# Kernel tuning notes

Hardware: AMD Instinct MI355X
Metric: run time of the kernel (lower is better)

Reference implementation:

```python
import jax, jax.numpy as jnp
import numpy as np

DECAY = 0.99   # LIF membrane decay
INH = 1.625    # lateral inhibition strength (mode='max')


def setup_inputs() -> dict:
    key = jax.random.key(0)
    kx, kw = jax.random.split(key)
    B, Cin, Cout = 8192, 4096, 1024
    x = (jax.random.uniform(kx, (B, Cin)) < 0.2).astype(jnp.float32)
    # weights, then normweight(): clamp to [0,1] and scale each row so row-max == 0.1
    W = jax.random.uniform(kw, (Cout, Cin), dtype=jnp.float32)
    W = W / (W.max(axis=1, keepdims=True) / 0.1)
    return {"x": x, "W": W, "time_window": 10}


def reference(x, W, time_window):
    # current through the bias-free linear layer; constant across timesteps
    i = x @ W.T                                   # (B, Cout)
    # adaptive threshold init: threshold = 3 * max over batch (thre_init branch)
    thr = 3.0 * i.max(axis=0)                     # (Cout,)
    imax = i.max(axis=1, keepdims=True)           # (B, 1), for mode='max' inhibition
    C = i.shape[1]

    def step(mem, _):
        mem = mem * DECAY + i                     # LIF integration
        s = (mem > thr).astype(i.dtype)           # threshold fire
        mem = mem * (1.0 - s)                     # hard reset at all spikers
        row = s.max(axis=1, keepdims=True)        # (B,1) 1 if any neuron in row spiked
        # winner-take-all k=1: keep a single spiking neuron per row (first/argmax)
        wta = jax.nn.one_hot(jnp.argmax(s, axis=1), C, dtype=i.dtype) * row
        # lateral inhibition: subtract inh * max-current from losers in rows that spiked
        mem = mem - INH * imax * (row - wta)
        return mem, wta

    mem0 = jnp.zeros_like(i)
    _, wtas = jax.lax.scan(step, mem0, None, length=time_window)
    return wtas.sum(axis=0)                       # accumulated spikes (B, Cout)
```

## Files before the change

kernel.cpp:

```cpp
#include <hip/hip_runtime.h>
#include <cstdint>

#define B_DIM 8192
#define CIN   4096
#define COUT  1024
#define NPLN  3072

constexpr double W_SCALE   = 83230720.0;
constexpr int    QMAX      = 8323072;
constexpr double INV_SCALE = 0.1 / 8323072.0;

using i32x4 = __attribute__((ext_vector_type(4))) int;

__device__ __forceinline__ void async_copy16(void* lds, const void* g) {
    auto l = (__attribute__((address_space(3))) void*)(uintptr_t)(lds);
    auto p = (const __attribute__((address_space(1))) void*)(uintptr_t)(g);
    __builtin_amdgcn_global_load_lds(p, l, 16, 0, 0);
}

__global__ void prep_x(const float* __restrict__ x, int8_t* __restrict__ Ai) {
    const int idx = blockIdx.x * 256 + threadIdx.x;
    const float4* xp = (const float4*)x + (size_t)idx * 4;
    float4 v0 = xp[0], v1 = xp[1], v2 = xp[2], v3 = xp[3];
    auto pk = [](float a, float b, float c, float d) -> int {
        return (a != 0.f ? 1 : 0) | ((b != 0.f ? 1 : 0) << 8) |
               ((c != 0.f ? 1 : 0) << 16) | ((d != 0.f ? 1 : 0) << 24);
    };
    int4 r;
    r.x = pk(v0.x, v0.y, v0.z, v0.w);
    r.y = pk(v1.x, v1.y, v1.z, v1.w);
    r.z = pk(v2.x, v2.y, v2.z, v2.w);
    r.w = pk(v3.x, v3.y, v3.z, v3.w);
    ((int4*)Ai)[idx] = r;
}

__global__ void prep_w(const float* __restrict__ W, int8_t* __restrict__ Bd,
                       unsigned long long* __restrict__ cm) {
    const int idx = blockIdx.x * 256 + threadIdx.x;
    float4 w = ((const float4*)W)[idx];
    float ws[4] = {w.x, w.y, w.z, w.w};
    char dg[3][4];
#pragma unroll
    for (int k = 0; k < 4; ++k) {
        int qv = __double2int_rn((double)ws[k] * W_SCALE);
        qv = max(0, min(QMAX, qv));
        int d0 = ((qv + 128) & 255) - 128; int tq = (qv - d0) >> 8;
        int d1 = ((tq + 128) & 255) - 128; int d2 = (tq - d1) >> 8;
        dg[0][k] = (char)d0; dg[1][k] = (char)d1; dg[2][k] = (char)d2;
    }
    const size_t off = (size_t)idx * 4;
#pragma unroll
    for (int p = 0; p < 3; ++p) {
        char4 c4; c4.x = dg[p][0]; c4.y = dg[p][1]; c4.z = dg[p][2]; c4.w = dg[p][3];
        *(char4*)(Bd + (size_t)p * COUT * CIN + off) = c4;
    }
    if (idx < COUT) cm[idx] = 0ull;
}

__global__ __launch_bounds__(256, 2) void gemm_i8(const int8_t* __restrict__ A,
                                                  const int8_t* __restrict__ Bm,
                                                  int* __restrict__ S) {
    __shared__ alignas(16) int8_t As[128 * 64];
    __shared__ alignas(16) int8_t Bs[128 * 64];
    const int tid  = threadIdx.x;
    const int lane = tid & 63;
    const int wave = tid >> 6;
    const int wr = wave >> 1, wc = wave & 1;
    const int bn = blockIdx.x, bm = blockIdx.y;

    const int r0  = tid >> 2;
    const int c0  = tid & 3;
    const int gc0 = c0 ^ ((r0 >> 1) & 3);
    const int r1  = r0 + 64;
    const int gc1 = c0 ^ ((r1 >> 1) & 3);
    const int8_t* Ag0 = A  + (size_t)(bm * 128 + r0) * CIN + gc0 * 16;
    const int8_t* Ag1 = A  + (size_t)(bm * 128 + r1) * CIN + gc1 * 16;
    const int8_t* Bg0 = Bm + (size_t)(bn * 128 + r0) * CIN + gc0 * 16;
    const int8_t* Bg1 = Bm + (size_t)(bn * 128 + r1) * CIN + gc1 * 16;
    int8_t* AsW = As + wave * 1024;
    int8_t* BsW = Bs + wave * 1024;

    const int mrow = lane & 15;
    const int q    = lane >> 4;
    const int sw   = (mrow >> 1) & 3;
    const int aoff = (wr * 64 + mrow) * 64 + (q ^ sw) * 16;
    const int boff = (wc * 64 + mrow) * 64 + (q ^ sw) * 16;

    i32x4 acc[4][4] = {};
    for (int kc = 0; kc < CIN; kc += 64) {
        __syncthreads();
        async_copy16(AsW,        Ag0 + kc);
        async_copy16(AsW + 4096, Ag1 + kc);
        async_copy16(BsW,        Bg0 + kc);
        async_copy16(BsW + 4096, Bg1 + kc);
        __syncthreads();
        i32x4 a[4], b[4];
#pragma unroll
        for (int t = 0; t < 4; ++t) a[t] = *(const i32x4*)(As + aoff + t * 1024);
#pragma unroll
        for (int t = 0; t < 4; ++t) b[t] = *(const i32x4*)(Bs + boff + t * 1024);
#pragma unroll
        for (int mt = 0; mt < 4; ++mt)
#pragma unroll
            for (int nt = 0; nt < 4; ++nt)
                acc[mt][nt] = __builtin_amdgcn_mfma_i32_16x16x64_i8(a[mt], b[nt], acc[mt][nt], 0, 0, 0);
    }

    const int gm0 = bm * 128 + wr * 64 + q * 4;
    const int gn0 = bn * 128 + wc * 64 + mrow;
#pragma unroll
    for (int mt = 0; mt < 4; ++mt)
#pragma unroll
        for (int nt = 0; nt < 4; ++nt) {
            const int gn = gn0 + nt * 16;
#pragma unroll
            for (int reg = 0; reg < 4; ++reg) {
                const int gm = gm0 + mt * 16 + reg;
                S[(size_t)gm * NPLN + gn] = acc[mt][nt][reg];
            }
        }
}

__global__ void colmax_k(const int* __restrict__ S, unsigned long long* __restrict__ cm) {
    const int j = blockIdx.x * 256 + threadIdx.x;
    const int rbeg = blockIdx.y * 128;
    double m = 0.0;
    for (int r = rbeg; r < rbeg + 128; ++r) {
        const int* row = S + (size_t)r * NPLN;
        long long s0 = row[j], s1 = row[COUT + j], s2 = row[2 * COUT + j];
        long long isum = s0 + s1 * 256 + s2 * 65536;
        double v = (double)isum * INV_SCALE;
        m = fmax(m, v);
    }
    atomicMax(cm + j, (unsigned long long)__double_as_longlong(m));
}

__global__ void scan_k(const int* __restrict__ S, const unsigned long long* __restrict__ cm,
                       const int* __restrict__ twp, float* __restrict__ out) {
    const int lane = threadIdx.x & 63;
    const int wave = threadIdx.x >> 6;
    const int b = blockIdx.x * 4 + wave;
    const int T = *twp;
    const int* row = S + (size_t)b * NPLN;

    double iv[16], mem[16], thr[16];
    int cnt[16];
    double imax = 0.0;
#pragma unroll
    for (int u = 0; u < 16; ++u) {
        const int j = lane + u * 64;
        long long s0 = row[j], s1 = row[COUT + j], s2 = row[2 * COUT + j];
        long long isum = s0 + s1 * 256 + s2 * 65536;
        iv[u]  = (double)isum * INV_SCALE;
        thr[u] = 3.0 * __longlong_as_double((long long)cm[j]);
        mem[u] = 0.0; cnt[u] = 0;
        imax = fmax(imax, iv[u]);
    }
#pragma unroll
    for (int d = 32; d >= 1; d >>= 1) imax = fmax(imax, __shfl_xor(imax, d, 64));
    const double h = 1.625 * imax;

    for (int t = 0; t < T; ++t) {
        int first = 0x7fffffff;
        bool sp[16];
#pragma unroll
        for (int u = 0; u < 16; ++u) {
            mem[u] = mem[u] * 0.99 + iv[u];
            sp[u] = mem[u] > thr[u];
            if (sp[u]) first = min(first, lane + u * 64);
        }
#pragma unroll
        for (int d = 32; d >= 1; d >>= 1) first = min(first, __shfl_xor(first, d, 64));
        const bool rowspike = first < 0x7fffffff;
#pragma unroll
        for (int u = 0; u < 16; ++u) {
            if (sp[u]) mem[u] = 0.0;
            if (rowspike) {
                if (lane + u * 64 == first) cnt[u]++;
                else mem[u] -= h;
            }
        }
    }
#pragma unroll
    for (int u = 0; u < 16; ++u)
        out[(size_t)b * COUT + lane + u * 64] = (float)cnt[u];
}

extern "C" void kernel_launch(void* const* d_in, const int* in_sizes, int n_in,
                              void* d_out, int out_size, void* d_ws, size_t ws_size,
                              hipStream_t stream) {
    const float* x  = (const float*)d_in[0];
    const float* W  = (const float*)d_in[1];
    const int*   tw = (const int*)d_in[2];
    float* out = (float*)d_out;

    int8_t* Ai = (int8_t*)d_ws;
    int8_t* Bd = Ai + (size_t)B_DIM * CIN;
    int*    S  = (int*)(Bd + (size_t)NPLN * CIN);
    unsigned long long* cm =
        (unsigned long long*)((int8_t*)S + (size_t)B_DIM * NPLN * 4);

    hipLaunchKernelGGL(prep_x,   dim3(8192),   dim3(256), 0, stream, x, Ai);
    hipLaunchKernelGGL(prep_w,   dim3(4096),   dim3(256), 0, stream, W, Bd, cm);
    hipLaunchKernelGGL(gemm_i8,  dim3(24, 64), dim3(256), 0, stream, Ai, Bd, S);
    hipLaunchKernelGGL(colmax_k, dim3(4, 64),  dim3(256), 0, stream, S, cm);
    hipLaunchKernelGGL(scan_k,   dim3(2048),   dim3(256), 0, stream, S, cm, tw, out);
}
```

Measured before the change: 391.6 us.

## Rewrite int8 GEMM with 256x256 tiles, double-buffered LDS pipeline and XCD-aware mapping

The int8 MFMA GEMM moves from 128x128 tiles with 4 waves and a load-then-compute loop to 256x256 tiles with 8 waves and 128-wide K chunks. A double-buffered 128KB LDS pipeline interleaves async global-to-LDS copies with MFMA quadrants, synchronised by explicit barriers, waitcnts and s_setprio. Workgroup ids are remapped across XCDs for L2 locality. The aim is to hide load latency and raise data reuse, at the cost of heavy LDS use, occupancy limits and fragile hand-counted waits.

After: 376.6 us. 1.04x faster.

```diff
diff --git a/kernel.cpp b/kernel.cpp
--- a/kernel.cpp
+++ b/kernel.cpp
@@ -57,68 +57,126 @@
     if (idx < COUT) cm[idx] = 0ull;
 }
 
-__global__ __launch_bounds__(256, 2) void gemm_i8(const int8_t* __restrict__ A,
+template <int MH, int NH>
+__device__ __forceinline__ void mma_quad(const i32x4 (&a)[4][2], const i32x4 (&b)[2][2],
+                                         i32x4 (&acc)[2][2][4][2]) {
+    __builtin_amdgcn_s_setprio(1);
+#pragma unroll
+    for (int mi = 0; mi < 4; ++mi)
+#pragma unroll
+        for (int ni = 0; ni < 2; ++ni)
+#pragma unroll
+            for (int kk = 0; kk < 2; ++kk)
+                acc[MH][NH][mi][ni] = __builtin_amdgcn_mfma_i32_16x16x64_i8(
+                    a[mi][kk], b[ni][kk], acc[MH][NH][mi][ni], 0, 0, 0);
+    __builtin_amdgcn_s_setprio(0);
+}
+
+#define BAR()   __builtin_amdgcn_s_barrier()
+#define LGKM0() asm volatile("s_waitcnt lgkmcnt(0)" ::: "memory")
+#define VMW(n)  asm volatile("s_waitcnt vmcnt(" #n ")" ::: "memory")
+
+__global__ __launch_bounds__(512, 2) void gemm_i8(const int8_t* __restrict__ A,
                                                   const int8_t* __restrict__ Bm,
                                                   int* __restrict__ S) {
-    __shared__ alignas(16) int8_t As[128 * 64];
-    __shared__ alignas(16) int8_t Bs[128 * 64];
+    __shared__ alignas(16) int8_t lds[131072];
     const int tid  = threadIdx.x;
     const int lane = tid & 63;
     const int wave = tid >> 6;
-    const int wr = wave >> 1, wc = wave & 1;
-    const int bn = blockIdx.x, bm = blockIdx.y;
-
-    const int r0  = tid >> 2;
-    const int c0  = tid & 3;
-    const int gc0 = c0 ^ ((r0 >> 1) & 3);
-    const int r1  = r0 + 64;
-    const int gc1 = c0 ^ ((r1 >> 1) & 3);
-    const int8_t* Ag0 = A  + (size_t)(bm * 128 + r0) * CIN + gc0 * 16;
-    const int8_t* Ag1 = A  + (size_t)(bm * 128 + r1) * CIN + gc1 * 16;
-    const int8_t* Bg0 = Bm + (size_t)(bn * 128 + r0) * CIN + gc0 * 16;
-    const int8_t* Bg1 = Bm + (size_t)(bn * 128 + r1) * CIN + gc1 * 16;
-    int8_t* AsW = As + wave * 1024;
-    int8_t* BsW = Bs + wave * 1024;
-
-    const int mrow = lane & 15;
-    const int q    = lane >> 4;
-    const int sw   = (mrow >> 1) & 3;
-    const int aoff = (wr * 64 + mrow) * 64 + (q ^ sw) * 16;
-    const int boff = (wc * 64 + mrow) * 64 + (q ^ sw) * 16;
-
-    i32x4 acc[4][4] = {};
-    for (int kc = 0; kc < CIN; kc += 64) {
-        __syncthreads();
-        async_copy16(AsW,        Ag0 + kc);
-        async_copy16(AsW + 4096, Ag1 + kc);
-        async_copy16(BsW,        Bg0 + kc);
-        async_copy16(BsW + 4096, Bg1 + kc);
-        __syncthreads();
-        i32x4 a[4], b[4];
-#pragma unroll
-        for (int t = 0; t < 4; ++t) a[t] = *(const i32x4*)(As + aoff + t * 1024);
-#pragma unroll
-        for (int t = 0; t < 4; ++t) b[t] = *(const i32x4*)(Bs + boff + t * 1024);
-#pragma unroll
-        for (int mt = 0; mt < 4; ++mt)
-#pragma unroll
-            for (int nt = 0; nt < 4; ++nt)
-                acc[mt][nt] = __builtin_amdgcn_mfma_i32_16x16x64_i8(a[mt], b[nt], acc[mt][nt], 0, 0, 0);
-    }
-
-    const int gm0 = bm * 128 + wr * 64 + q * 4;
-    const int gn0 = bn * 128 + wc * 64 + mrow;
-#pragma unroll
-    for (int mt = 0; mt < 4; ++mt)
-#pragma unroll
-        for (int nt = 0; nt < 4; ++nt) {
-            const int gn = gn0 + nt * 16;
-#pragma unroll
-            for (int reg = 0; reg < 4; ++reg) {
-                const int gm = gm0 + mt * 16 + reg;
-                S[(size_t)gm * NPLN + gn] = acc[mt][nt][reg];
-            }
-        }
+
+    const int wg = ((int)blockIdx.x & 7) * 48 + ((int)blockIdx.x >> 3);
+    const int bm = wg & 31;
+    const int bn = wg >> 5;
+
+    const int stid   = tid >> 3;
+    const int cswz16 = ((tid & 7) ^ (stid & 7)) << 4;
+    const int8_t* gA = A  + (size_t)(bm * 256 + stid) * CIN + cswz16;
+    const int8_t* gB = Bm + (size_t)(bn * 256 + stid) * CIN + cswz16;
+    const int wv1024 = wave << 10;
+
+#define STAGE_A(t_, hs_) do {                                                   \
+    int8_t* d_ = lds + (((t_) & 1) << 15) + ((hs_) << 14) + wv1024;             \
+    const int8_t* s_ = gA + (size_t)((hs_) * 128) * CIN + ((t_) << 7);          \
+    async_copy16(d_,        s_);                                                \
+    async_copy16(d_ + 8192, s_ + (size_t)64 * CIN);                             \
+} while (0)
+#define STAGE_B(t_, hs_) do {                                                   \
+    int8_t* d_ = lds + 65536 + (((t_) & 1) << 15) + ((hs_) << 14) + wv1024;     \
+    const int8_t* s_ = gB + (size_t)((hs_) * 128) * CIN + ((t_) << 7);          \
+    async_copy16(d_,        s_);                                                \
+    async_copy16(d_ + 8192, s_ + (size_t)64 * CIN);                             \
+} while (0)
+
+    const int wr = wave >> 2, wc = wave & 3;
+    const int fr = lane & 15;
+    const int q  = lane >> 4;
+    const int ck0 = (q ^ (lane & 7)) << 4;
+    const int ck1 = ck0 ^ 64;
+    const int abase = (wr * 64 + fr) * 128;
+    const int bbase = 65536 + (wc * 32 + fr) * 128;
+
+    i32x4 a[4][2], b0[2][2], b1[2][2];
+    i32x4 acc[2][2][4][2] = {};
+
+#define LDA(buf_, mh_) do {                                                     \
+    const int8_t* p_ = lds + ((buf_) << 15) + ((mh_) << 14) + abase;            \
+    a[0][0] = *(const i32x4*)(p_ + ck0);        a[0][1] = *(const i32x4*)(p_ + ck1);        \
+    a[1][0] = *(const i32x4*)(p_ + 2048 + ck0); a[1][1] = *(const i32x4*)(p_ + 2048 + ck1); \
+    a[2][0] = *(const i32x4*)(p_ + 4096 + ck0); a[2][1] = *(const i32x4*)(p_ + 4096 + ck1); \
+    a[3][0] = *(const i32x4*)(p_ + 6144 + ck0); a[3][1] = *(const i32x4*)(p_ + 6144 + ck1); \
+} while (0)
+#define LDB(arr_, buf_, nh_) do {                                               \
+    const int8_t* p_ = lds + ((buf_) << 15) + ((nh_) << 14) + bbase;            \
+    arr_[0][0] = *(const i32x4*)(p_ + ck0);        arr_[0][1] = *(const i32x4*)(p_ + ck1);        \
+    arr_[1][0] = *(const i32x4*)(p_ + 2048 + ck0); arr_[1][1] = *(const i32x4*)(p_ + 2048 + ck1); \
+} while (0)
+
+    STAGE_A(0, 0); STAGE_B(0, 0); STAGE_B(0, 1); STAGE_A(0, 1);
+    STAGE_A(1, 0); STAGE_B(1, 0);
+    VMW(8); BAR();
+
+#pragma unroll 1
+    for (int it = 0; it < 15; ++it) {
+        const int t = it * 2;
+        LDA(0, 0); LDB(b0, 0, 0); STAGE_B(t + 1, 1); BAR(); LGKM0(); mma_quad<0, 0>(a, b0, acc); VMW(8); BAR();
+        LDB(b1, 0, 1);            STAGE_A(t + 1, 1); BAR(); LGKM0(); mma_quad<0, 1>(a, b1, acc); VMW(8); BAR();
+        LDA(0, 1);                STAGE_A(t + 2, 0); BAR(); LGKM0(); mma_quad<1, 0>(a, b0, acc); VMW(8); BAR();
+                                  STAGE_B(t + 2, 0); BAR(); LGKM0(); mma_quad<1, 1>(a, b1, acc); VMW(8); BAR();
+        LDA(1, 0); LDB(b0, 1, 0); STAGE_B(t + 2, 1); BAR(); LGKM0(); mma_quad<0, 0>(a, b0, acc); VMW(8); BAR();
+        LDB(b1, 1, 1);            STAGE_A(t + 2, 1); BAR(); LGKM0(); mma_quad<0, 1>(a, b1, acc); VMW(8); BAR();
+        LDA(1, 1);                STAGE_A(t + 3, 0); BAR(); LGKM0(); mma_quad<1, 0>(a, b0, acc); VMW(8); BAR();
+                                  STAGE_B(t + 3, 0); BAR(); LGKM0(); mma_quad<1, 1>(a, b1, acc); VMW(8); BAR();
+    }
+    LDA(0, 0); LDB(b0, 0, 0); STAGE_B(31, 1); BAR(); LGKM0(); mma_quad<0, 0>(a, b0, acc); VMW(8); BAR();
+    LDB(b1, 0, 1);            STAGE_A(31, 1); BAR(); LGKM0(); mma_quad<0, 1>(a, b1, acc); VMW(8); BAR();
+    LDA(0, 1);                                BAR(); LGKM0(); mma_quad<1, 0>(a, b0, acc); VMW(8); BAR();
+                                              BAR(); LGKM0(); mma_quad<1, 1>(a, b1, acc); VMW(4); BAR();
+    LDA(1, 0); LDB(b0, 1, 0);                 BAR(); LGKM0(); mma_quad<0, 0>(a, b0, acc); VMW(2); BAR();
+    LDB(b1, 1, 1);                            BAR(); LGKM0(); mma_quad<0, 1>(a, b1, acc); VMW(0); BAR();
+    LDA(1, 1);                                BAR(); LGKM0(); mma_quad<1, 0>(a, b0, acc);
+                                                              mma_quad<1, 1>(a, b1, acc);
+
+    const int gm0 = bm * 256 + wr * 64 + q * 4;
+    const int gn0 = bn * 256 + wc * 32 + fr;
+#pragma unroll
+    for (int mh = 0; mh < 2; ++mh)
+#pragma unroll
+        for (int nh = 0; nh < 2; ++nh)
+#pragma unroll
+            for (int mi = 0; mi < 4; ++mi)
+#pragma unroll
+                for (int ni = 0; ni < 2; ++ni) {
+                    const int gn = gn0 + nh * 128 + ni * 16;
+#pragma unroll
+                    for (int reg = 0; reg < 4; ++reg) {
+                        const int gm = gm0 + mh * 128 + mi * 16 + reg;
+                        S[(size_t)gm * NPLN + gn] = acc[mh][nh][mi][ni][reg];
+                    }
+                }
+#undef STAGE_A
+#undef STAGE_B
+#undef LDA
+#undef LDB
 }
 
 __global__ void colmax_k(const int* __restrict__ S, unsigned long long* __restrict__ cm) {
@@ -200,9 +258,9 @@
     unsigned long long* cm =
         (unsigned long long*)((int8_t*)S + (size_t)B_DIM * NPLN * 4);
 
-    hipLaunchKernelGGL(prep_x,   dim3(8192),   dim3(256), 0, stream, x, Ai);
-    hipLaunchKernelGGL(prep_w,   dim3(4096),   dim3(256), 0, stream, W, Bd, cm);
-    hipLaunchKernelGGL(gemm_i8,  dim3(24, 64), dim3(256), 0, stream, Ai, Bd, S);
-    hipLaunchKernelGGL(colmax_k, dim3(4, 64),  dim3(256), 0, stream, S, cm);
-    hipLaunchKernelGGL(scan_k,   dim3(2048),   dim3(256), 0, stream, S, cm, tw, out);
-}
+    hipLaunchKernelGGL(prep_x,   dim3(8192),  dim3(256), 0, stream, x, Ai);
+    hipLaunchKernelGGL(prep_w,   dim3(4096),  dim3(256), 0, stream, W, Bd, cm);
+    hipLaunchKernelGGL(gemm_i8,  dim3(384),   dim3(512), 0, stream, Ai, Bd, S);
+    hipLaunchKernelGGL(colmax_k, dim3(4, 64), dim3(256), 0, stream, S, cm);
+    hipLaunchKernelGGL(scan_k,   dim3(2048),  dim3(256), 0, stream, S, cm, tw, out);
+}
```

## Fuse digit-plane recombination and column max into pipelined 512-thread int8 GEMM

Applied to the files above, without the earlier changes.

Rewrites the int8 GEMM so each 512-thread block computes a 128x256 output tile for all three weight digit planes, accumulating them in registers. Loads are double-buffered through 128KB of LDS with explicit waitcnt and barrier scheduling, and MFMA sections are wrapped in setprio. The epilogue recombines the planes into double values, writes a single double matrix, and folds the column max into the GEMM through an LDS reduction plus atomicMax, which removes the colmax kernel and the three-plane int32 intermediate. In exchange it adds register pressure (48 accumulator vectors) and a large LDS footprint that limits occupancy.

Result: faster. 345.5 us (-11.8%).

```diff
diff --git a/kernel.cpp b/kernel.cpp
--- a/kernel.cpp
+++ b/kernel.cpp
@@ -4,7 +4,6 @@
 #define B_DIM 8192
 #define CIN   4096
 #define COUT  1024
-#define NPLN  3072
 
 constexpr double W_SCALE   = 83230720.0;
 constexpr int    QMAX      = 8323072;
@@ -57,91 +56,160 @@
     if (idx < COUT) cm[idx] = 0ull;
 }
 
-__global__ __launch_bounds__(256, 2) void gemm_i8(const int8_t* __restrict__ A,
+template <int P>
+__device__ __forceinline__ void mma16(const i32x4 (&a)[4], const i32x4 (&b)[4],
+                                      i32x4 (&acc)[3][4][4]) {
+    __builtin_amdgcn_s_setprio(1);
+#pragma unroll
+    for (int mi = 0; mi < 4; ++mi)
+#pragma unroll
+        for (int ni = 0; ni < 4; ++ni)
+            acc[P][mi][ni] = __builtin_amdgcn_mfma_i32_16x16x64_i8(
+                a[mi], b[ni], acc[P][mi][ni], 0, 0, 0);
+    __builtin_amdgcn_s_setprio(0);
+}
+
+#define BAR()   __builtin_amdgcn_s_barrier()
+#define LGKM0() asm volatile("s_waitcnt lgkmcnt(0)" ::: "memory")
+#define VMW(n)  asm volatile("s_waitcnt vmcnt(" #n ")" ::: "memory")
+
+__global__ __launch_bounds__(512, 2) void gemm_i8(const int8_t* __restrict__ A,
                                                   const int8_t* __restrict__ Bm,
-                                                  int* __restrict__ S) {
-    __shared__ alignas(16) int8_t As[128 * 64];
-    __shared__ alignas(16) int8_t Bs[128 * 64];
+                                                  double* __restrict__ Sc,
+                                                  unsigned long long* __restrict__ cm) {
+    __shared__ alignas(16) int8_t lds[131072];
     const int tid  = threadIdx.x;
     const int lane = tid & 63;
     const int wave = tid >> 6;
-    const int wr = wave >> 1, wc = wave & 1;
-    const int bn = blockIdx.x, bm = blockIdx.y;
-
-    const int r0  = tid >> 2;
-    const int c0  = tid & 3;
-    const int gc0 = c0 ^ ((r0 >> 1) & 3);
-    const int r1  = r0 + 64;
-    const int gc1 = c0 ^ ((r1 >> 1) & 3);
-    const int8_t* Ag0 = A  + (size_t)(bm * 128 + r0) * CIN + gc0 * 16;
-    const int8_t* Ag1 = A  + (size_t)(bm * 128 + r1) * CIN + gc1 * 16;
-    const int8_t* Bg0 = Bm + (size_t)(bn * 128 + r0) * CIN + gc0 * 16;
-    const int8_t* Bg1 = Bm + (size_t)(bn * 128 + r1) * CIN + gc1 * 16;
-    int8_t* AsW = As + wave * 1024;
-    int8_t* BsW = Bs + wave * 1024;
-
-    const int mrow = lane & 15;
-    const int q    = lane >> 4;
-    const int sw   = (mrow >> 1) & 3;
-    const int aoff = (wr * 64 + mrow) * 64 + (q ^ sw) * 16;
-    const int boff = (wc * 64 + mrow) * 64 + (q ^ sw) * 16;
-
-    i32x4 acc[4][4] = {};
-    for (int kc = 0; kc < CIN; kc += 64) {
-        __syncthreads();
-        async_copy16(AsW,        Ag0 + kc);
-        async_copy16(AsW + 4096, Ag1 + kc);
-        async_copy16(BsW,        Bg0 + kc);
-        async_copy16(BsW + 4096, Bg1 + kc);
-        __syncthreads();
-        i32x4 a[4], b[4];
-#pragma unroll
-        for (int t = 0; t < 4; ++t) a[t] = *(const i32x4*)(As + aoff + t * 1024);
-#pragma unroll
-        for (int t = 0; t < 4; ++t) b[t] = *(const i32x4*)(Bs + boff + t * 1024);
-#pragma unroll
-        for (int mt = 0; mt < 4; ++mt)
-#pragma unroll
-            for (int nt = 0; nt < 4; ++nt)
-                acc[mt][nt] = __builtin_amdgcn_mfma_i32_16x16x64_i8(a[mt], b[nt], acc[mt][nt], 0, 0, 0);
-    }
+
+    const int wg = (int)blockIdx.x;
+    const int bn = wg & 3;
+    const int bm = wg >> 2;
+
+    const int stid   = tid >> 3;
+    const int cswz16 = ((tid & 7) ^ (stid & 7)) << 4;
+    const int8_t* gA = A  + (size_t)(bm * 128 + stid) * CIN + cswz16;
+    const int8_t* gB = Bm + (size_t)(bn * 256 + stid) * CIN + cswz16;
+    const int wv1024 = wave << 10;
+
+#define SA_(t_) do {                                                            \
+    int8_t* d_ = lds + (((t_) & 1) << 14) + wv1024;                             \
+    const int8_t* s_ = gA + ((t_) << 7);                                        \
+    async_copy16(d_,        s_);                                                \
+    async_copy16(d_ + 8192, s_ + (size_t)64 * CIN);                             \
+} while (0)
+#define SB_(t_, p_) do {                                                        \
+    int8_t* d_ = lds + 32768 + ((p_) << 15) + wv1024;                           \
+    const int8_t* s_ = gB + (size_t)(p_) * COUT * CIN + ((t_) << 7);            \
+    async_copy16(d_,         s_);                                               \
+    async_copy16(d_ + 8192,  s_ + (size_t)64  * CIN);                           \
+    async_copy16(d_ + 16384, s_ + (size_t)128 * CIN);                           \
+    async_copy16(d_ + 24576, s_ + (size_t)192 * CIN);                           \
+} while (0)
+
+    const int wr = wave >> 2, wc = wave & 3;
+    const int fr = lane & 15;
+    const int q  = lane >> 4;
+    const int ck0 = (q ^ (fr & 7)) << 4;
+    const int abase = (wr * 64 + fr) * 128;
+    const int bbase = (wc * 64 + fr) * 128;
+
+    i32x4 a[4], b[4];
+    i32x4 acc[3][4][4] = {};
+
+#define LDA_(t_, kk_) do {                                                      \
+    const int8_t* p_ = lds + (((t_) & 1) << 14) + abase + (ck0 ^ ((kk_) * 64)); \
+    a[0] = *(const i32x4*)(p_);        a[1] = *(const i32x4*)(p_ + 2048);       \
+    a[2] = *(const i32x4*)(p_ + 4096); a[3] = *(const i32x4*)(p_ + 6144);       \
+} while (0)
+#define LDB_(p_, kk_) do {                                                      \
+    const int8_t* q_ = lds + 32768 + ((p_) << 15) + bbase + (ck0 ^ ((kk_) * 64)); \
+    b[0] = *(const i32x4*)(q_);        b[1] = *(const i32x4*)(q_ + 2048);       \
+    b[2] = *(const i32x4*)(q_ + 4096); b[3] = *(const i32x4*)(q_ + 6144);       \
+} while (0)
+
+    SA_(0); SB_(0, 0); SB_(0, 1);
+    VMW(4); BAR();
+
+#pragma unroll 1
+    for (int t = 0; t < 31; ++t) {
+        LDA_(t, 0); LDB_(0, 0); SB_(t, 2); SA_(t + 1);
+        BAR(); LGKM0(); mma16<0>(a, b, acc); VMW(6); BAR();
+        LDB_(1, 0);
+        BAR(); LGKM0(); mma16<1>(a, b, acc); VMW(2); BAR();
+        LDB_(2, 0);
+        BAR(); LGKM0(); mma16<2>(a, b, acc); BAR();
+        LDA_(t, 1); LDB_(0, 1);
+        BAR(); LGKM0(); mma16<0>(a, b, acc); BAR();
+        LDB_(1, 1); SB_(t + 1, 0);
+        BAR(); LGKM0(); mma16<1>(a, b, acc); BAR();
+        LDB_(2, 1); SB_(t + 1, 1);
+        BAR(); LGKM0(); mma16<2>(a, b, acc); VMW(4); BAR();
+    }
+    LDA_(31, 0); LDB_(0, 0); SB_(31, 2);
+    BAR(); LGKM0(); mma16<0>(a, b, acc); VMW(4); BAR();
+    LDB_(1, 0);
+    BAR(); LGKM0(); mma16<1>(a, b, acc); VMW(0); BAR();
+    LDB_(2, 0);
+    BAR(); LGKM0(); mma16<2>(a, b, acc); BAR();
+    LDA_(31, 1); LDB_(0, 1);
+    BAR(); LGKM0(); mma16<0>(a, b, acc); BAR();
+    LDB_(1, 1);
+    BAR(); LGKM0(); mma16<1>(a, b, acc); BAR();
+    LDB_(2, 1);
+    BAR(); LGKM0(); mma16<2>(a, b, acc); BAR();
 
     const int gm0 = bm * 128 + wr * 64 + q * 4;
-    const int gn0 = bn * 128 + wc * 64 + mrow;
-#pragma unroll
-    for (int mt = 0; mt < 4; ++mt)
-#pragma unroll
-        for (int nt = 0; nt < 4; ++nt) {
-            const int gn = gn0 + nt * 16;
+    const int gn0 = bn * 256 + wc * 64 + fr;
+    double vmax[4] = {0.0, 0.0, 0.0, 0.0};
+#pragma unroll
+    for (int mi = 0; mi < 4; ++mi)
+#pragma unroll
+        for (int ni = 0; ni < 4; ++ni) {
+            const int gn = gn0 + ni * 16;
 #pragma unroll
             for (int reg = 0; reg < 4; ++reg) {
-                const int gm = gm0 + mt * 16 + reg;
-                S[(size_t)gm * NPLN + gn] = acc[mt][nt][reg];
+                const int gm = gm0 + mi * 16 + reg;
+                long long isum = (long long)acc[0][mi][ni][reg]
+                               + 256ll   * (long long)acc[1][mi][ni][reg]
+                               + 65536ll * (long long)acc[2][mi][ni][reg];
+                double v = (double)isum * INV_SCALE;
+                Sc[(size_t)gm * COUT + gn] = v;
+                vmax[ni] = fmax(vmax[ni], v);
             }
         }
-}
-
-__global__ void colmax_k(const int* __restrict__ S, unsigned long long* __restrict__ cm) {
-    const int j = blockIdx.x * 256 + threadIdx.x;
-    const int rbeg = blockIdx.y * 128;
-    double m = 0.0;
-    for (int r = rbeg; r < rbeg + 128; ++r) {
-        const int* row = S + (size_t)r * NPLN;
-        long long s0 = row[j], s1 = row[COUT + j], s2 = row[2 * COUT + j];
-        long long isum = s0 + s1 * 256 + s2 * 65536;
-        double v = (double)isum * INV_SCALE;
-        m = fmax(m, v);
-    }
-    atomicMax(cm + j, (unsigned long long)__double_as_longlong(m));
-}
-
-__global__ void scan_k(const int* __restrict__ S, const unsigned long long* __restrict__ cm,
+#pragma unroll
+    for (int ni = 0; ni < 4; ++ni) {
+        vmax[ni] = fmax(vmax[ni], __shfl_xor(vmax[ni], 16, 64));
+        vmax[ni] = fmax(vmax[ni], __shfl_xor(vmax[ni], 32, 64));
+    }
+    double* red = (double*)lds;
+    if (lane < 16) {
+#pragma unroll
+        for (int ni = 0; ni < 4; ++ni)
+            red[wave * 64 + ni * 16 + fr] = vmax[ni];
+    }
+    __syncthreads();
+    if (tid < 256) {
+        const int c = tid;
+        const int wcq = c >> 6, nic = (c >> 4) & 3, frc = c & 15;
+        double m = fmax(red[wcq * 64 + nic * 16 + frc],
+                        red[(wcq + 4) * 64 + nic * 16 + frc]);
+        atomicMax(cm + bn * 256 + c, (unsigned long long)__double_as_longlong(m));
+    }
+#undef SA_
+#undef SB_
+#undef LDA_
+#undef LDB_
+}
+
+__global__ void scan_k(const double* __restrict__ Sc, const unsigned long long* __restrict__ cm,
                        const int* __restrict__ twp, float* __restrict__ out) {
     const int lane = threadIdx.x & 63;
     const int wave = threadIdx.x >> 6;
     const int b = blockIdx.x * 4 + wave;
     const int T = *twp;
-    const int* row = S + (size_t)b * NPLN;
+    const double* row = Sc + (size_t)b * COUT;
 
     double iv[16], mem[16], thr[16];
     int cnt[16];
@@ -149,9 +217,7 @@
 #pragma unroll
     for (int u = 0; u < 16; ++u) {
         const int j = lane + u * 64;
-        long long s0 = row[j], s1 = row[COUT + j], s2 = row[2 * COUT + j];
-        long long isum = s0 + s1 * 256 + s2 * 65536;
-        iv[u]  = (double)isum * INV_SCALE;
+        iv[u]  = row[j];
         thr[u] = 3.0 * __longlong_as_double((long long)cm[j]);
         mem[u] = 0.0; cnt[u] = 0;
         imax = fmax(imax, iv[u]);
@@ -196,13 +262,12 @@
 
     int8_t* Ai = (int8_t*)d_ws;
     int8_t* Bd = Ai + (size_t)B_DIM * CIN;
-    int*    S  = (int*)(Bd + (size_t)NPLN * CIN);
+    double* Sc = (double*)(Bd + (size_t)3 * COUT * CIN);
     unsigned long long* cm =
-        (unsigned long long*)((int8_t*)S + (size_t)B_DIM * NPLN * 4);
-
-    hipLaunchKernelGGL(prep_x,   dim3(8192),   dim3(256), 0, stream, x, Ai);
-    hipLaunchKernelGGL(prep_w,   dim3(4096),   dim3(256), 0, stream, W, Bd, cm);
-    hipLaunchKernelGGL(gemm_i8,  dim3(24, 64), dim3(256), 0, stream, Ai, Bd, S);
-    hipLaunchKernelGGL(colmax_k, dim3(4, 64),  dim3(256), 0, stream, S, cm);
-    hipLaunchKernelGGL(scan_k,   dim3(2048),   dim3(256), 0, stream, S, cm, tw, out);
-}
+        (unsigned long long*)((int8_t*)Sc + (size_t)B_DIM * COUT * 8);
+
+    hipLaunchKernelGGL(prep_x,  dim3(8192), dim3(256), 0, stream, x, Ai);
+    hipLaunchKernelGGL(prep_w,  dim3(4096), dim3(256), 0, stream, W, Bd, cm);
+    hipLaunchKernelGGL(gemm_i8, dim3(256),  dim3(512), 0, stream, Ai, Bd, Sc, cm);
+    hipLaunchKernelGGL(scan_k,  dim3(2048), dim3(256), 0, stream, Sc, cm, tw, out);
+}
```
